# Performance work log

Hardware: AMD Instinct MI355X
Metric: run time of the kernel (lower is better)

The kernel has to match this reference:

```python
import jax, jax.numpy as jnp
import numpy as np
from jax import lax

H, P, N, G, K, CHUNK = 64, 64, 128, 1, 4, 256
D_MODEL = 2048
D_INNER = H * P            # 4096
CONV_DIM = D_INNER + 2 * G * N  # 4352
EPS = 1e-5


def setup_inputs() -> dict:
    key = jax.random.key(0)
    ks = jax.random.split(key, 6)
    s = lambda k, shape, scale: jax.random.normal(k, shape, jnp.float32) * scale
    return {
        "hidden_states": s(ks[0], (2, 2048, D_MODEL), 1.0),
        "in_proj_w": s(ks[1], (D_MODEL, D_INNER + CONV_DIM + H), D_MODEL ** -0.5),
        "conv_w": s(ks[2], (CONV_DIM, K), K ** -0.5),
        "conv_b": jnp.zeros((CONV_DIM,), jnp.float32),
        "dt_bias": jnp.ones((H,), jnp.float32),
        "A_log": jnp.log(jnp.arange(1, H + 1, dtype=jnp.float32)),
        "D_param": jnp.ones((H,), jnp.float32),
        "norm_w": jnp.ones((D_INNER,), jnp.float32),
        "out_proj_w": s(ks[3], (D_INNER, D_MODEL), D_INNER ** -0.5),
    }


def _mamba2_forward(hidden_states, in_proj_w, conv_w, conv_b, dt_bias, A_log, D_param, norm_w, out_proj_w):
    b, l, _ = hidden_states.shape
    c = l // CHUNK  # number of chunks

    # in_proj -> gate | conv channels (x,B,C) | dt
    proj = hidden_states @ in_proj_w
    gate = proj[..., :D_INNER]
    hbc = proj[..., D_INNER:D_INNER + CONV_DIM]
    dt = proj[..., D_INNER + CONV_DIM:]  # [b,l,H]

    # depthwise causal conv1d + silu
    xt = hbc.transpose(0, 2, 1)  # [b, CONV_DIM, l]
    y = lax.conv_general_dilated(
        xt, conv_w[:, None, :], window_strides=(1,), padding=[(K - 1, 0)],
        feature_group_count=CONV_DIM, dimension_numbers=("NCH", "OIH", "NCH"))
    hbc = jax.nn.silu(y + conv_b[None, :, None]).transpose(0, 2, 1)  # [b,l,CONV_DIM]

    # split into x / B / C per group (unflatten over groups as in torch code)
    per_g = D_INNER // G
    hg = hbc.reshape(b, l, G, per_g + 2 * N)
    x = hg[..., :per_g].reshape(b, l, H, P)                 # [b,l,h,p]
    Bm = hg[..., per_g:per_g + N]                            # [b,l,g,n]
    Cm = hg[..., per_g + N:]                                 # [b,l,g,n]
    hpg = H // G
    Bh = jnp.repeat(Bm, hpg, axis=2)                         # [b,l,h,n]
    Ch = jnp.repeat(Cm, hpg, axis=2)

    # dt: softplus(dt + bias), clamp per time_step_limit (0, inf)
    dt = jax.nn.softplus(dt + dt_bias)                       # [b,l,h]
    A = -jnp.exp(A_log)                                      # [h]

    # chunk the sequence
    x_c = x.reshape(b, c, CHUNK, H, P)
    B_c = Bh.reshape(b, c, CHUNK, H, N)
    C_c = Ch.reshape(b, c, CHUNK, H, N)
    dt_c = dt.reshape(b, c, CHUNK, H)

    dA = dt_c * A[None, None, None, :]                       # [b,c,L,h]
    cum = jnp.cumsum(dA, axis=2)                             # [b,c,L,h]

    # intra-chunk (diagonal block): decay[i,j] = exp(cum_i - cum_j), i>=j
    diff = cum[:, :, :, None, :] - cum[:, :, None, :, :]     # [b,c,i,j,h]
    i = jnp.arange(CHUNK)
    mask = i[:, None] >= i[None, :]
    decay = jnp.exp(jnp.where(mask[None, None, :, :, None], diff, -jnp.inf))
    scores = jnp.einsum("bcihn,bcjhn->bcijh", C_c, B_c) * decay * dt_c[:, :, None, :, :]
    Y_diag = jnp.einsum("bcijh,bcjhp->bcihp", scores, x_c)   # [b,c,L,h,p]

    # per-chunk final states
    decay_states = jnp.exp(cum[:, :, -1:, :] - cum)          # [b,c,L,h]
    states = jnp.einsum("bclh,bclhn,bclhp->bchpn", decay_states * dt_c, B_c, x_c)
    chunk_decay = jnp.exp(cum[:, :, -1, :])                  # [b,c,h]

    # inter-chunk recurrence over chunks
    def step(prev, inp):
        st, cd = inp  # [b,h,p,n], [b,h]
        new = cd[:, :, None, None] * prev + st
        return new, prev

    init = jnp.zeros((b, H, P, N), hidden_states.dtype)
    _, prev_states = lax.scan(step, init, (jnp.moveaxis(states, 1, 0), jnp.moveaxis(chunk_decay, 1, 0)))
    prev_states = jnp.moveaxis(prev_states, 0, 1)            # [b,c,h,p,n]

    state_decay_out = jnp.exp(cum)                           # [b,c,L,h]
    Y_off = jnp.einsum("bclhn,bchpn,bclh->bclhp", C_c, prev_states, state_decay_out)

    yh = (Y_diag + Y_off).reshape(b, l, H, P) + D_param[None, None, :, None] * x
    yr = yh.reshape(b, l, D_INNER)

    # gated RMSNorm
    hidden = yr * jax.nn.silu(gate)
    var = jnp.mean(hidden * hidden, axis=-1, keepdims=True)
    hidden = hidden * lax.rsqrt(var + EPS) * norm_w

    return hidden @ out_proj_w


def reference(hidden_states, in_proj_w, conv_w, conv_b, dt_bias, A_log, D_param, norm_w, out_proj_w):
    return _mamba2_forward(hidden_states, in_proj_w, conv_w, conv_b, dt_bias, A_log, D_param, norm_w, out_proj_w)
```

## Files before the change

### kernel.cpp

```cpp
#include <hip/hip_runtime.h>
#include <hip/hip_bf16.h>


typedef __attribute__((ext_vector_type(8))) _Float16 f16x8;
typedef __attribute__((ext_vector_type(4))) float f32x4;

#define GLD16(gp, lp) __builtin_amdgcn_global_load_lds( \
    (__attribute__((address_space(1))) void*)(gp),      \
    (__attribute__((address_space(3))) void*)(lp), 16, 0, 0)

__device__ __forceinline__ unsigned short f2h(float v) {
  _Float16 h = (_Float16)v;
  return *reinterpret_cast<unsigned short*>(&h);
}
__device__ __forceinline__ float h2f(unsigned short u) {
  _Float16 h = *reinterpret_cast<_Float16*>(&u);
  return (float)h;
}
__device__ __forceinline__ float siluf(float x) { return x / (1.f + expf(-x)); }

__global__ __launch_bounds__(256) void prep(const float* __restrict__ hs,
                                            const float* __restrict__ Win,
                                            _Float16* __restrict__ Ah,
                                            _Float16* __restrict__ WtH,
                                            float* __restrict__ zf) {
  __shared__ __attribute__((aligned(16))) char smemP[32768];
  const int bid = blockIdx.x;
  const int tid = threadIdx.x;
  if (bid < 1024) {
    float (*Xs)[2048] = reinterpret_cast<float (*)[2048]>(smemP);
    int t0 = bid * 4;
#pragma unroll
    for (int i = 0; i < 8; i++) {
      int e = tid * 4 + i * 1024;
      int tok = e >> 11, k = e & 2047;
      *reinterpret_cast<float4*>(&Xs[tok][k]) =
          *reinterpret_cast<const float4*>(&hs[(long)(t0 + tok) * 2048 + k]);
    }
    __syncthreads();
    int h = tid & 63, tg = tid >> 6;
    float a0 = 0.f, a1 = 0.f, a2 = 0.f, a3 = 0.f;
    const float* wcol = Win + 8448 + h;
    for (int k = 0; k < 2048; k += 4) {
      a0 = fmaf(Xs[tg][k + 0], wcol[(long)(k + 0) * 8512], a0);
      a1 = fmaf(Xs[tg][k + 1], wcol[(long)(k + 1) * 8512], a1);
      a2 = fmaf(Xs[tg][k + 2], wcol[(long)(k + 2) * 8512], a2);
      a3 = fmaf(Xs[tg][k + 3], wcol[(long)(k + 3) * 8512], a3);
    }
    zf[(long)(t0 + tg) * 64 + h] = (a0 + a1) + (a2 + a3);
  } else if (bid < 9216) {
    long i = ((long)(bid - 1024) * 256 + tid) * 4;
    float4 v = *reinterpret_cast<const float4*>(hs + i);
    ushort4 u;
    u.x = f2h(v.x); u.y = f2h(v.y); u.z = f2h(v.z); u.w = f2h(v.w);
    *reinterpret_cast<ushort4*>((unsigned short*)Ah + i) = u;
  } else {
    float (*tile)[33] = reinterpret_cast<float (*)[33]>(smemP);
    int i = bid - 9216;
    int c0 = (i % 264) * 32, r0 = (i / 264) * 32;
    int tx = tid & 31, ty = tid >> 5;
#pragma unroll
    for (int j = 0; j < 4; j++)
      tile[ty + j * 8][tx] = Win[(long)(r0 + ty + j * 8) * 8512 + c0 + tx];
    __syncthreads();
#pragma unroll
    for (int j = 0; j < 4; j++) {
      int c = c0 + ty + j * 8, r = r0 + tx;
      WtH[(long)c * 2048 + r] = (_Float16)tile[tx][ty + j * 8];
    }
  }
}

__global__ __launch_bounds__(512, 2) void gemm_in8(const _Float16* __restrict__ A,
                                                   const _Float16* __restrict__ Bt,
                                                   _Float16* __restrict__ gate,
                                                   float* __restrict__ hbcf,
                                                   float* __restrict__ rparts) {
  __shared__ __attribute__((aligned(128))) char ldsB[131072];
  const int tid = threadIdx.x;
  const int lane = tid & 63;
  const int wv = tid >> 6;
  const int wr = wv >> 2, wc = wv & 3;
  const int wg = blockIdx.x;
  const bool rem = wg >= 512;
  int by, bxn, kbase, zz;
  if (!rem) {
    const int xcd = wg & 7, j = wg >> 3;
    by = (xcd >> 2) * 8 + (j >> 3);
    bxn = (xcd & 3) * 8 + (j & 7);
    kbase = 0; zz = 0;
  } else {
    const int idx = wg - 512;
    by = idx & 15; zz = idx >> 4; bxn = 32; kbase = zz * 256;
  }

  const int srow = tid >> 3;
  const int scolg = (tid & 7) ^ (srow & 7);
  const _Float16* Ab = A + (long)by * 524288 + (long)srow * 2048 + scolg * 8 + kbase;
  const _Float16* Bb = Bt + (long)bxn * 524288 + (long)srow * 2048 + scolg * 8 + kbase;
  const int ldst = tid << 4;

#define STAGE_A(tau, h) do {                                              \
    const _Float16* g_ = Ab + (long)(h) * 262144 + (tau) * 64;            \
    char* l_ = ldsB + ((((tau) & 1) << 2) + (h)) * 16384 + ldst;          \
    GLD16(g_, l_); GLD16(g_ + 131072, l_ + 8192); } while (0)
#define STAGE_B(tau, h) do {                                              \
    const _Float16* g_ = Bb + (long)(h) * 262144 + (tau) * 64;            \
    char* l_ = ldsB + ((((tau) & 1) << 2) + 2 + (h)) * 16384 + ldst;      \
    GLD16(g_, l_); GLD16(g_ + 131072, l_ + 8192); } while (0)

  const int fr = lane & 15;
  const int c16 = (lane >> 4) ^ (fr & 7);
  const int aOff0 = wr * 16384 + fr * 128 + c16 * 16;
  const int aOff1 = aOff0 ^ 64;
  const int bOff0 = (2 + (wc >> 1)) * 16384 + ((wc & 1) * 64 + fr) * 128 + c16 * 16;
  const int bOff1 = bOff0 ^ 64;
#define RD_A(b, mi, k32) (*(const f16x8*)(ldsB + ((k32) ? aOff1 : aOff0) + (b) * 65536 + (mi) * 2048))
#define RD_B(b, ni, k32) (*(const f16x8*)(ldsB + ((k32) ? bOff1 : bOff0) + (b) * 65536 + (ni) * 2048))

#define BAR() __builtin_amdgcn_s_barrier()
#define WLG0() asm volatile("s_waitcnt lgkmcnt(0)" ::: "memory")
#define WLG8() asm volatile("s_waitcnt lgkmcnt(8)" ::: "memory")
#define WVM4() asm volatile("s_waitcnt vmcnt(4)" ::: "memory")

  f32x4 acc[8][4];
#pragma unroll
  for (int mi = 0; mi < 8; ++mi)
#pragma unroll
    for (int ni = 0; ni < 4; ++ni) acc[mi][ni] = f32x4{0.f, 0.f, 0.f, 0.f};

  STAGE_A(0, 0); STAGE_A(0, 1); STAGE_B(0, 0); STAGE_B(0, 1);
  STAGE_B(1, 0); STAGE_B(1, 1);
  WVM4(); BAR();

#define MFMA_Q(MI0, MI1, x0, x1, x2, x3, PB)                                        \
  __builtin_amdgcn_s_setprio(1);                                                    \
  _Pragma("unroll") for (int ni = 0; ni < 4; ++ni) {                                \
    acc[MI0][ni] = __builtin_amdgcn_mfma_f32_16x16x32_f16(x0, PB[ni][0], acc[MI0][ni], 0, 0, 0); \
    acc[MI0][ni] = __builtin_amdgcn_mfma_f32_16x16x32_f16(x1, PB[ni][1], acc[MI0][ni], 0, 0, 0); \
    acc[MI1][ni] = __builtin_amdgcn_mfma_f32_16x16x32_f16(x2, PB[ni][0], acc[MI1][ni], 0, 0, 0); \
    acc[MI1][ni] = __builtin_amdgcn_mfma_f32_16x16x32_f16(x3, PB[ni][1], acc[MI1][ni], 0, 0, 0); \
  }                                                                                 \
  __builtin_amdgcn_s_setprio(0);

#define ITER8(u, msk) do {                                                          \
    const int t1 = (2 * (u) + 1) & (msk);                                           \
    const int t2 = (2 * (u) + 2) & (msk);                                           \
    const int t3 = (2 * (u) + 3) & (msk);                                           \
    f16x8 PB0[4][2];                                                                \
    _Pragma("unroll") for (int ni = 0; ni < 4; ++ni) {                              \
      PB0[ni][0] = RD_B(0, ni, 0); PB0[ni][1] = RD_B(0, ni, 1); }                   \
    {                                                                               \
      f16x8 x0 = RD_A(0, 0, 0), x1 = RD_A(0, 0, 1), x2 = RD_A(0, 1, 0), x3 = RD_A(0, 1, 1); \
      STAGE_A(t1, 0); WLG8(); BAR(); WLG0();                                        \
      MFMA_Q(0, 1, x0, x1, x2, x3, PB0) BAR();                                      \
    }                                                                               \
    {                                                                               \
      f16x8 x0 = RD_A(0, 2, 0), x1 = RD_A(0, 2, 1), x2 = RD_A(0, 3, 0), x3 = RD_A(0, 3, 1); \
      STAGE_A(t1, 1); BAR(); WLG0();                                                \
      MFMA_Q(2, 3, x0, x1, x2, x3, PB0) BAR();                                      \
    }                                                                               \
    {                                                                               \
      f16x8 x0 = RD_A(0, 4, 0), x1 = RD_A(0, 4, 1), x2 = RD_A(0, 5, 0), x3 = RD_A(0, 5, 1); \
      STAGE_B(t2, 0); BAR(); WLG0();                                                \
      MFMA_Q(4, 5, x0, x1, x2, x3, PB0) BAR();                                      \
    }                                                                               \
    {                                                                               \
      f16x8 x0 = RD_A(0, 6, 0), x1 = RD_A(0, 6, 1), x2 = RD_A(0, 7, 0), x3 = RD_A(0, 7, 1); \
      STAGE_B(t2, 1); BAR(); WLG0();                                                \
      MFMA_Q(6, 7, x0, x1, x2, x3, PB0) WVM4(); BAR();                              \
    }                                                                               \
    f16x8 PB1[4][2];                                                                \
    _Pragma("unroll") for (int ni = 0; ni < 4; ++ni) {                              \
      PB1[ni][0] = RD_B(1, ni, 0); PB1[ni][1] = RD_B(1, ni, 1); }                   \
    {                                                                               \
      f16x8 x0 = RD_A(1, 0, 0), x1 = RD_A(1, 0, 1), x2 = RD_A(1, 1, 0), x3 = RD_A(1, 1, 1); \
      STAGE_A(t2, 0); WLG8(); BAR(); WLG0();                                        \
      MFMA_Q(0, 1, x0, x1, x2, x3, PB1) BAR();                                      \
    }                                                                               \
    {                                                                               \
      f16x8 x0 = RD_A(1, 2, 0), x1 = RD_A(1, 2, 1), x2 = RD_A(1, 3, 0), x3 = RD_A(1, 3, 1); \
      STAGE_A(t2, 1); BAR(); WLG0();                                                \
      MFMA_Q(2, 3, x0, x1, x2, x3, PB1) BAR();                                      \
    }                                                                               \
    {                                                                               \
      f16x8 x0 = RD_A(1, 4, 0), x1 = RD_A(1, 4, 1), x2 = RD_A(1, 5, 0), x3 = RD_A(1, 5, 1); \
      STAGE_B(t3, 0); BAR(); WLG0();                                                \
      MFMA_Q(4, 5, x0, x1, x2, x3, PB1) BAR();                                      \
    }                                                                               \
    {                                                                               \
      f16x8 x0 = RD_A(1, 6, 0), x1 = RD_A(1, 6, 1), x2 = RD_A(1, 7, 0), x3 = RD_A(1, 7, 1); \
      STAGE_B(t3, 1); BAR(); WLG0();                                                \
      MFMA_Q(6, 7, x0, x1, x2, x3, PB1) WVM4(); BAR();                              \
    }                                                                               \
  } while (0)

  if (!rem) {
    for (int u = 0; u < 16; ++u) ITER8(u, 31);
  } else {
    for (int u = 0; u < 2; ++u) ITER8(u, 3);
  }

  const int m0 = by * 256 + wr * 128;
  const int cl = lane & 15, rq = (lane >> 4) * 4;
  if (!rem) {
    const int n0 = bxn * 256 + wc * 64;
    if (bxn < 16) {
#pragma unroll
      for (int mi = 0; mi < 8; ++mi)
#pragma unroll
        for (int r = 0; r < 4; ++r) {
          long rowoff = (long)(m0 + mi * 16 + rq + r) * 4096 + n0 + cl;
#pragma unroll
          for (int ni = 0; ni < 4; ++ni) gate[rowoff + ni * 16] = (_Float16)acc[mi][ni][r];
        }
    } else {
#pragma unroll
      for (int mi = 0; mi < 8; ++mi)
#pragma unroll
        for (int r = 0; r < 4; ++r) {
          long rowoff = (long)(m0 + mi * 16 + rq + r) * 4352 + (n0 - 4096) + cl;
#pragma unroll
          for (int ni = 0; ni < 4; ++ni) hbcf[rowoff + ni * 16] = acc[mi][ni][r];
        }
    }
  } else {
    float* rp = rparts + (long)zz * 1048576;
    const int ncol = wc * 64;
#pragma unroll
    for (int mi = 0; mi < 8; ++mi)
#pragma unroll
      for (int r = 0; r < 4; ++r) {
        long rowoff = (long)(m0 + mi * 16 + rq + r) * 256 + ncol + cl;
#pragma unroll
        for (int ni = 0; ni < 4; ++ni) rp[rowoff + ni * 16] = acc[mi][ni][r];
      }
  }
#undef STAGE_A
#undef STAGE_B
#undef RD_A
#undef RD_B
#undef ITER8
}

__global__ __launch_bounds__(256) void fuse2(const float* __restrict__ zf,
                                             const float* __restrict__ dtb,
                                             const float* __restrict__ Alog,
                                             float* __restrict__ dt_f,
                                             float* __restrict__ cum_f,
                                             float* __restrict__ cuml,
                                             const float* __restrict__ rp,
                                             float* __restrict__ hbcf,
                                             const float* __restrict__ Wout,
                                             _Float16* __restrict__ WoutT) {
  __shared__ __attribute__((aligned(16))) char smem2[4352];
  const int bid = blockIdx.x;
  const int tid = threadIdx.x;
  if (bid < 16) {
    float (*segsum)[64] = reinterpret_cast<float (*)[64]>(smem2);
    int bc = bid;
    int h = tid & 63, seg = tid >> 6;
    int t0 = bc * 256;
    float Ah = -expf(Alog[h]);
    float bias = dtb[h];
    float s = 0.f;
    for (int j = 0; j < 64; j++) {
      int t = t0 + seg * 64 + j;
      float z = zf[(long)t * 64 + h] + bias;
      float v = (z > 20.f) ? z : log1pf(expf(z));
      dt_f[(long)t * 64 + h] = v;
      s += v * Ah;
    }
    segsum[seg][h] = s;
    __syncthreads();
    float run = 0.f;
    for (int k = 0; k < seg; k++) run += segsum[k][h];
    for (int j = 0; j < 64; j++) {
      int t = t0 + seg * 64 + j;
      run += dt_f[(long)t * 64 + h] * Ah;
      cum_f[(long)t * 64 + h] = run;
    }
    if (seg == 3) cuml[bc * 64 + h] = run;
  } else if (bid < 1040) {
    long e = ((long)(bid - 16) * 256 + tid) * 4;
    float4 s = *reinterpret_cast<const float4*>(rp + e);
#pragma unroll
    for (int z = 1; z < 8; ++z) {
      float4 v = *reinterpret_cast<const float4*>(rp + (long)z * 1048576 + e);
      s.x += v.x; s.y += v.y; s.z += v.z; s.w += v.w;
    }
    long row = e >> 8, col = e & 255;
    *reinterpret_cast<float4*>(hbcf + row * 4352 + 4096 + col) = s;
  } else {
    float (*tile)[33] = reinterpret_cast<float (*)[33]>(smem2);
    int i = bid - 1040;
    int c0 = (i & 63) * 32, r0 = (i >> 6) * 32;
    int tx = tid & 31, ty = tid >> 5;
#pragma unroll
    for (int j = 0; j < 4; j++)
      tile[ty + j * 8][tx] = Wout[(long)(r0 + ty + j * 8) * 2048 + c0 + tx];
    __syncthreads();
#pragma unroll
    for (int j = 0; j < 4; j++) {
      int c = c0 + ty + j * 8, r = r0 + tx;
      WoutT[(long)c * 4096 + r] = (_Float16)tile[tx][ty + j * 8];
    }
  }
}

__global__ __launch_bounds__(256) void convx(const float* __restrict__ hbcf,
                                             const float* __restrict__ convw,
                                             const float* __restrict__ convb,
                                             _Float16* __restrict__ x16,
                                             _Float16* __restrict__ B16,
                                             _Float16* __restrict__ C16,
                                             unsigned short* __restrict__ xT16) {
  __shared__ unsigned short tile[64][66];
  const int bx = blockIdx.x, t0 = blockIdx.y * 64;
  const int tid = threadIdx.x;
  const int tq = tid & 63, tg = tid >> 6;
  const int q0 = (bx < 64) ? bx * 64 : 4096 + (bx - 64) * 64;
  const int q = q0 + tq;
  const int ts = t0 + tg * 16;
  const int bstart = ts & ~2047;
  const float* colq = hbcf + q;
  float4 wq = *reinterpret_cast<const float4*>(convw + q * 4);
  float bconv = convb[q];
  float v3 = (ts - 3 >= bstart) ? colq[(long)(ts - 3) * 4352] : 0.f;
  float v2 = (ts - 2 >= bstart) ? colq[(long)(ts - 2) * 4352] : 0.f;
  float v1 = (ts - 1 >= bstart) ? colq[(long)(ts - 1) * 4352] : 0.f;
  if (bx < 64) {
#pragma unroll
    for (int j = 0; j < 16; ++j) {
      int t = ts + j;
      float v0 = colq[(long)t * 4352];
      float a = bconv + v3 * wq.x + v2 * wq.y + v1 * wq.z + v0 * wq.w;
      unsigned short o = f2h(siluf(a));
      ((unsigned short*)x16)[(long)t * 4096 + q] = o;
      tile[tg * 16 + j][tq] = o;
      v3 = v2; v2 = v1; v1 = v0;
    }
    __syncthreads();
    int tx = tid & 15, ty = tid >> 4;
#pragma unroll
    for (int i = 0; i < 4; ++i) {
      int c = ty + i * 16;
      ushort4 v;
      v.x = tile[4 * tx + 0][c]; v.y = tile[4 * tx + 1][c];
      v.z = tile[4 * tx + 2][c]; v.w = tile[4 * tx + 3][c];
      *(ushort4*)&xT16[(long)(q0 + c) * 4096 + t0 + 4 * tx] = v;
    }
  } else {
#pragma unroll
    for (int j = 0; j < 16; ++j) {
      int t = ts + j;
      float v0 = colq[(long)t * 4352];
      float a = bconv + v3 * wq.x + v2 * wq.y + v1 * wq.z + v0 * wq.w;
      _Float16 o = (_Float16)siluf(a);
      if (q < 4224) B16[(long)t * 128 + (q - 4096)] = o;
      else C16[(long)t * 128 + (q - 4224)] = o;
      v3 = v2; v2 = v1; v1 = v0;
    }
  }
}

__global__ __launch_bounds__(256) void fuse3(const unsigned short* __restrict__ xT16,
                                             const _Float16* __restrict__ B16,
                                             const _Float16* __restrict__ C16,
                                             const float* __restrict__ dt_f,
                                             const float* __restrict__ cum_f,
                                             const float* __restrict__ cuml,
                                             float* __restrict__ states,
                                             float* __restrict__ CBT,
                                             float* __restrict__ ssq) {
  __shared__ __attribute__((aligned(16))) char smem3[16384];
  const int bid = blockIdx.x;
  const int tid = threadIdx.x;
  const int wv = tid >> 6, lane = tid & 63;
  const int mr = lane & 15, koff = (lane >> 4) * 8;
  if (bid < 1024) {
    float* w_s = (float*)smem3;
    unsigned short* Aw = (unsigned short*)(smem3 + 1024);
    unsigned short* BT = (unsigned short*)(smem3 + 6144);
    int h = bid & 63, bc = bid >> 6;
    int t0 = bc * 256;
    {
      int t = t0 + tid;
      w_s[tid] = expf(cuml[bc * 64 + h] - cum_f[(long)t * 64 + h]) * dt_f[(long)t * 64 + h];
    }
    __syncthreads();
    f32x4 acc[4][2];
#pragma unroll
    for (int mi = 0; mi < 4; mi++)
#pragma unroll
      for (int nj = 0; nj < 2; nj++) acc[mi][nj] = f32x4{0.f, 0.f, 0.f, 0.f};
    for (int kt = 0; kt < 8; kt++) {
      {
        int p = tid >> 2, tq2 = tid & 3;
        const unsigned short* g = &xT16[((long)(h * 64 + p)) * 4096 + t0 + kt * 32 + tq2 * 8];
        ushort4 u0 = *(const ushort4*)g, u1 = *(const ushort4*)(g + 4);
        const float* wp = &w_s[kt * 32 + tq2 * 8];
        ushort4 o0, o1;
        o0.x = f2h(h2f(u0.x) * wp[0]); o0.y = f2h(h2f(u0.y) * wp[1]);
        o0.z = f2h(h2f(u0.z) * wp[2]); o0.w = f2h(h2f(u0.w) * wp[3]);
        o1.x = f2h(h2f(u1.x) * wp[4]); o1.y = f2h(h2f(u1.y) * wp[5]);
        o1.z = f2h(h2f(u1.z) * wp[6]); o1.w = f2h(h2f(u1.w) * wp[7]);
        *(ushort4*)&Aw[p * 40 + tq2 * 8] = o0;
        *(ushort4*)&Aw[p * 40 + tq2 * 8 + 4] = o1;
      }
      {
        int tl = tid >> 3, ng = tid & 7;
        const unsigned short* g = (const unsigned short*)B16 +
                                  ((long)(t0 + kt * 32 + tl)) * 128 + ng * 16;
#pragma unroll
        for (int j = 0; j < 16; j++) BT[(ng * 16 + j) * 40 + tl] = g[j];
      }
      __syncthreads();
      f16x8 af[4], bf[2];
#pragma unroll
      for (int mi = 0; mi < 4; mi++)
        af[mi] = *(const f16x8*)&Aw[(mi * 16 + mr) * 40 + koff];
#pragma unroll
      for (int nj = 0; nj < 2; nj++)
        bf[nj] = *(const f16x8*)&BT[((wv * 2 + nj) * 16 + mr) * 40 + koff];
#pragma unroll
      for (int mi = 0; mi < 4; mi++)
#pragma unroll
        for (int nj = 0; nj < 2; nj++)
          acc[mi][nj] = __builtin_amdgcn_mfma_f32_16x16x32_f16(af[mi], bf[nj],
                                                               acc[mi][nj], 0, 0, 0);
      __syncthreads();
    }
    int cl = lane & 15, rq = (lane >> 4) * 4;
    long base = ((long)(bc * 64 + h)) * 8192;
#pragma unroll
    for (int mi = 0; mi < 4; mi++)
#pragma unroll
      for (int r = 0; r < 4; r++) {
        int p = mi * 16 + rq + r;
#pragma unroll
        for (int nj = 0; nj < 2; nj++) {
          int n = (wv * 2 + nj) * 16 + cl;
          states[base + p * 128 + n] = acc[mi][nj][r];
        }
      }
  } else if (bid < 1088) {
    _Float16* As = (_Float16*)smem3;
    _Float16* Bs = (_Float16*)(smem3 + 8192);
    int i = bid - 1024;
    int bx = i & 1, by = (i >> 1) & 1, bz = i >> 2;
    const _Float16* Ab = C16 + (long)bz * 32768 + (long)by * 128 * 128;
    const _Float16* Bb = B16 + (long)bz * 32768 + (long)bx * 128 * 128;
    const int c0 = wv * 128 + lane;
    const int c1 = c0 + 64;
    const long ra0 = (long)(c0 >> 2) * 128 + (c0 & 3) * 8;
    const long ra1 = (long)(c1 >> 2) * 128 + (c1 & 3) * 8;
    f32x4 acc[4][4];
#pragma unroll
    for (int mi = 0; mi < 4; mi++)
#pragma unroll
      for (int ni = 0; ni < 4; ni++) acc[mi][ni] = f32x4{0.f, 0.f, 0.f, 0.f};
    const int mrow = (wv & 1) * 64 + (lane & 15);
    const int nrow = (wv >> 1) * 64 + (lane & 15);
    for (int k0 = 0; k0 < 128; k0 += 32) {
      GLD16(Ab + ra0 + k0, (char*)As + c0 * 16);
      GLD16(Ab + ra1 + k0, (char*)As + c1 * 16);
      GLD16(Bb + ra0 + k0, (char*)Bs + c0 * 16);
      GLD16(Bb + ra1 + k0, (char*)Bs + c1 * 16);
      __syncthreads();
      f16x8 af[4], bfr[4];
#pragma unroll
      for (int mi = 0; mi < 4; mi++)
        af[mi] = *(const f16x8*)(As + (mrow + mi * 16) * 32 + koff);
#pragma unroll
      for (int ni = 0; ni < 4; ni++)
        bfr[ni] = *(const f16x8*)(Bs + (nrow + ni * 16) * 32 + koff);
#pragma unroll
      for (int mi = 0; mi < 4; mi++)
#pragma unroll
        for (int ni = 0; ni < 4; ni++)
          acc[mi][ni] = __builtin_amdgcn_mfma_f32_16x16x32_f16(af[mi], bfr[ni],
                                                               acc[mi][ni], 0, 0, 0);
      __syncthreads();
    }
    const int m0 = by * 128 + (wv & 1) * 64;
    const int n0 = bx * 128 + (wv >> 1) * 64;
    const int cl = lane & 15, rq = (lane >> 4) * 4;
    const long zc = (long)bz * 65536;
#pragma unroll
    for (int mi = 0; mi < 4; mi++)
#pragma unroll
      for (int r = 0; r < 4; r++) {
        long rowoff = zc + (long)(m0 + mi * 16 + rq + r) * 256 + n0 + cl;
#pragma unroll
        for (int ni = 0; ni < 4; ni++) CBT[rowoff + ni * 16] = acc[mi][ni][r];
      }
  } else {
    int i = (bid - 1088) * 1024 + tid * 4;
    *reinterpret_cast<float4*>(&ssq[i]) = make_float4(0.f, 0.f, 0.f, 0.f);
  }
}

__global__ __launch_bounds__(256) void recur_kernel(float* __restrict__ states,
                                                    const float* __restrict__ cuml) {
  int g = blockIdx.x;
  int bh = g >> 3, js = g & 7;
  int b = bh >> 6, h = bh & 63;
  int tid = threadIdx.x;
  float4 prev = make_float4(0.f, 0.f, 0.f, 0.f);
  for (int c = 0; c < 8; c++) {
    int bc = b * 8 + c;
    float cd = expf(cuml[bc * 64 + h]);
    long o = (long)(bc * 64 + h) * 8192 + js * 1024 + tid * 4;
    float4 st = *reinterpret_cast<const float4*>(&states[o]);
    *reinterpret_cast<float4*>(&states[o]) = prev;
    prev.x = fmaf(cd, prev.x, st.x);
    prev.y = fmaf(cd, prev.y, st.y);
    prev.z = fmaf(cd, prev.z, st.z);
    prev.w = fmaf(cd, prev.w, st.w);
  }
}

__global__ __launch_bounds__(256, 4) void yfused(const unsigned short* __restrict__ xT16,
                                                 const unsigned short* __restrict__ x16,
                                                 const unsigned short* __restrict__ C16,
                                                 const unsigned short* __restrict__ gate,
                                                 const float* __restrict__ CBT,
                                                 const float* __restrict__ states,
                                                 const float* __restrict__ dt_f,
                                                 const float* __restrict__ cum_f,
                                                 const float* __restrict__ Dp,
                                                 unsigned short* __restrict__ hid,
                                                 float* __restrict__ ssq) {
  int h = blockIdx.x, bc = blockIdx.y;
  int t0 = bc * 256, tid = threadIdx.x;
  __shared__ unsigned short Sb[256 * 40];
  __shared__ unsigned short PS[64 * 136];
  __shared__ float cum_s[256], dt_s[256];
  int i = tid;
  cum_s[i] = cum_f[(long)(t0 + i) * 64 + h];
  dt_s[i] = dt_f[(long)(t0 + i) * 64 + h];
  {
    int p = tid >> 2, nq = tid & 3;
    const float* g = &states[((long)(bc * 64 + h)) * 8192 + p * 128 + nq * 32];
    unsigned short* l = &PS[p * 136 + nq * 32];
#pragma unroll
    for (int c = 0; c < 8; c++) {
      float4 v = *(const float4*)(g + c * 4);
      ushort4 u;
      u.x = f2h(v.x); u.y = f2h(v.y); u.z = f2h(v.z); u.w = f2h(v.w);
      *(ushort4*)(l + c * 4) = u;
    }
  }
  __syncthreads();
  float cum_i = cum_s[i];
  const float* cbrow = CBT + (long)bc * 65536 + (long)i * 256;
  int wv = tid >> 6, lane = tid & 63;
  int mr = lane & 15, koff = (lane >> 4) * 8;
  const unsigned short* xTb = xT16 + ((long)(h * 64 + mr)) * 4096 + t0 + koff;
  f32x4 acc[4][4];
#pragma unroll
  for (int mi = 0; mi < 4; mi++)
#pragma unroll
    for (int ni = 0; ni < 4; ni++) acc[mi][ni] = f32x4{0.f, 0.f, 0.f, 0.f};
  const int ktmax = 2 * wv + 2;
  for (int kt = 0; kt < ktmax; kt++) {
    int k0 = kt * 32;
    f16x8 bf[4];
#pragma unroll
    for (int ni = 0; ni < 4; ni++)
      bf[ni] = *(const f16x8*)(xTb + (long)(ni * 16) * 4096 + k0);
#pragma unroll
    for (int c = 0; c < 8; c++) {
      float4 cb = *(const float4*)&cbrow[k0 + c * 4];
      ushort4 o;
      {
        int j = k0 + c * 4 + 0;
        float s = (j <= i) ? cb.x * expf(cum_i - cum_s[j]) * dt_s[j] : 0.f;
        o.x = f2h(s);
      }
      {
        int j = k0 + c * 4 + 1;
        float s = (j <= i) ? cb.y * expf(cum_i - cum_s[j]) * dt_s[j] : 0.f;
        o.y = f2h(s);
      }
      {
        int j = k0 + c * 4 + 2;
        float s = (j <= i) ? cb.z * expf(cum_i - cum_s[j]) * dt_s[j] : 0.f;
        o.z = f2h(s);
      }
      {
        int j = k0 + c * 4 + 3;
        float s = (j <= i) ? cb.w * expf(cum_i - cum_s[j]) * dt_s[j] : 0.f;
        o.w = f2h(s);
      }
      *(ushort4*)&Sb[i * 40 + c * 4] = o;
    }
    f16x8 af[4];
#pragma unroll
    for (int mi = 0; mi < 4; mi++)
      af[mi] = *(const f16x8*)&Sb[(64 * wv + mi * 16 + mr) * 40 + koff];
#pragma unroll
    for (int mi = 0; mi < 4; mi++)
#pragma unroll
      for (int ni = 0; ni < 4; ni++)
        acc[mi][ni] = __builtin_amdgcn_mfma_f32_16x16x32_f16(af[mi], bf[ni],
                                                             acc[mi][ni], 0, 0, 0);
  }
  float fac_i = expf(cum_i);
  for (int kn = 0; kn < 4; kn++) {
    {
      const unsigned short* g = &C16[((long)(t0 + i)) * 128 + kn * 32];
#pragma unroll
      for (int c = 0; c < 8; c++) {
        ushort4 u = *(const ushort4*)(g + c * 4);
        ushort4 o;
        o.x = f2h(h2f(u.x) * fac_i); o.y = f2h(h2f(u.y) * fac_i);
        o.z = f2h(h2f(u.z) * fac_i); o.w = f2h(h2f(u.w) * fac_i);
        *(ushort4*)&Sb[i * 40 + c * 4] = o;
      }
    }
    f16x8 af[4], bf[4];
#pragma unroll
    for (int mi = 0; mi < 4; mi++)
      af[mi] = *(const f16x8*)&Sb[(64 * wv + mi * 16 + mr) * 40 + koff];
#pragma unroll
    for (int ni = 0; ni < 4; ni++)
      bf[ni] = *(const f16x8*)&PS[(ni * 16 + mr) * 136 + kn * 32 + koff];
#pragma unroll
    for (int mi = 0; mi < 4; mi++)
#pragma unroll
      for (int ni = 0; ni < 4; ni++)
        acc[mi][ni] = __builtin_amdgcn_mfma_f32_16x16x32_f16(af[mi], bf[ni],
                                                             acc[mi][ni], 0, 0, 0);
  }
  float Dh = Dp[h];
  int cl = lane & 15, rq = (lane >> 4) * 4;
#pragma unroll
  for (int mi = 0; mi < 4; mi++)
#pragma unroll
    for (int r = 0; r < 4; r++) {
      long row = t0 + 64 * wv + mi * 16 + rq + r;
      const unsigned short* xr = &x16[row * 4096 + h * 64];
      const unsigned short* gr = &gate[row * 4096 + h * 64];
      unsigned short* hw = &hid[row * 4096 + h * 64];
      float ssp = 0.f;
#pragma unroll
      for (int ni = 0; ni < 4; ni++) {
        int p = ni * 16 + cl;
        float yv = acc[mi][ni][r] + Dh * h2f(xr[p]);
        float hv = yv * siluf(h2f(gr[p]));
        hw[p] = f2h(hv);
        ssp += hv * hv;
      }
#pragma unroll
      for (int o = 8; o > 0; o >>= 1) ssp += __shfl_down(ssp, o, 16);
      if (cl == 0) atomicAdd(&ssq[row], ssp);
    }
}

__global__ __launch_bounds__(256) void scale_kernel(const float* __restrict__ ssq,
                                                    const float* __restrict__ nw,
                                                    unsigned short* __restrict__ hid) {
  int row = blockIdx.x;
  int tid = threadIdx.x;
  float sc = rsqrtf(ssq[row] * (1.f / 4096.f) + 1e-5f);
  unsigned short* hp = hid + (long)row * 4096;
  int d0 = tid * 16;
#pragma unroll
  for (int c = 0; c < 4; c++) {
    int d = d0 + c * 4;
    ushort4 u = *reinterpret_cast<ushort4*>(&hp[d]);
    float4 w = *reinterpret_cast<const float4*>(&nw[d]);
    u.x = f2h(h2f(u.x) * sc * w.x);
    u.y = f2h(h2f(u.y) * sc * w.y);
    u.z = f2h(h2f(u.z) * sc * w.z);
    u.w = f2h(h2f(u.w) * sc * w.w);
    *reinterpret_cast<ushort4*>(&hp[d]) = u;
  }
}

__global__ __launch_bounds__(512, 2) void gemm_out8(const _Float16* __restrict__ A,
                                                    const _Float16* __restrict__ Bt,
                                                    float* __restrict__ Cp0,
                                                    float* __restrict__ Cp1) {
  __shared__ __attribute__((aligned(128))) char ldsB[131072];
  const int tid = threadIdx.x;
  const int lane = tid & 63;
  const int wv = tid >> 6;
  const int wr = wv >> 2, wc = wv & 3;
  const int wg = blockIdx.x;
  const int xcd = wg & 7, j = wg >> 3;
  const int z = j >> 4, t = j & 15;
  const int by = (xcd >> 1) * 4 + (t >> 2);
  const int bx = (xcd & 1) * 4 + (t & 3);

  const int srow = tid >> 3;
  const int scolg = (tid & 7) ^ (srow & 7);
  const _Float16* Ab = A + (long)by * 256 * 4096 + (long)z * 2048 +
                       (long)srow * 4096 + scolg * 8;
  const _Float16* Bb = Bt + (long)bx * 256 * 4096 + (long)z * 2048 +
                       (long)srow * 4096 + scolg * 8;
  const int ldst = tid << 4;

#define STAGE_A(tau, h) do {                                              \
    const _Float16* g_ = Ab + (long)(h) * 524288 + (tau) * 64;            \
    char* l_ = ldsB + ((((tau) & 1) << 2) + (h)) * 16384 + ldst;          \
    GLD16(g_, l_); GLD16(g_ + 262144, l_ + 8192); } while (0)
#define STAGE_B(tau, h) do {                                              \
    const _Float16* g_ = Bb + (long)(h) * 524288 + (tau) * 64;            \
    char* l_ = ldsB + ((((tau) & 1) << 2) + 2 + (h)) * 16384 + ldst;      \
    GLD16(g_, l_); GLD16(g_ + 262144, l_ + 8192); } while (0)

  const int fr = lane & 15;
  const int c16 = (lane >> 4) ^ (fr & 7);
  const int aOff0 = wr * 16384 + fr * 128 + c16 * 16;
  const int aOff1 = aOff0 ^ 64;
  const int bOff0 = (2 + (wc >> 1)) * 16384 + ((wc & 1) * 64 + fr) * 128 + c16 * 16;
  const int bOff1 = bOff0 ^ 64;
#define RD_A(b, mi, k32) (*(const f16x8*)(ldsB + ((k32) ? aOff1 : aOff0) + (b) * 65536 + (mi) * 2048))
#define RD_B(b, ni, k32) (*(const f16x8*)(ldsB + ((k32) ? bOff1 : bOff0) + (b) * 65536 + (ni) * 2048))

#define BAR() __builtin_amdgcn_s_barrier()
#define WLG0() asm volatile("s_waitcnt lgkmcnt(0)" ::: "memory")
#define WLG8() asm volatile("s_waitcnt lgkmcnt(8)" ::: "memory")
#define WVM4() asm volatile("s_waitcnt vmcnt(4)" ::: "memory")

  f32x4 acc[8][4];
#pragma unroll
  for (int mi = 0; mi < 8; ++mi)
#pragma unroll
    for (int ni = 0; ni < 4; ++ni) acc[mi][ni] = f32x4{0.f, 0.f, 0.f, 0.f};

  STAGE_A(0, 0); STAGE_A(0, 1); STAGE_B(0, 0); STAGE_B(0, 1);
  STAGE_B(1, 0); STAGE_B(1, 1);
  WVM4(); BAR();

#define MFMA_Q(MI0, MI1, x0, x1, x2, x3, PB)                                        \
  __builtin_amdgcn_s_setprio(1);                                                    \
  _Pragma("unroll") for (int ni = 0; ni < 4; ++ni) {                                \
    acc[MI0][ni] = __builtin_amdgcn_mfma_f32_16x16x32_f16(x0, PB[ni][0], acc[MI0][ni], 0, 0, 0); \
    acc[MI0][ni] = __builtin_amdgcn_mfma_f32_16x16x32_f16(x1, PB[ni][1], acc[MI0][ni], 0, 0, 0); \
    acc[MI1][ni] = __builtin_amdgcn_mfma_f32_16x16x32_f16(x2, PB[ni][0], acc[MI1][ni], 0, 0, 0); \
    acc[MI1][ni] = __builtin_amdgcn_mfma_f32_16x16x32_f16(x3, PB[ni][1], acc[MI1][ni], 0, 0, 0); \
  }                                                                                 \
  __builtin_amdgcn_s_setprio(0);

  for (int u = 0; u < 16; ++u) {
    const int t1 = 2 * u + 1;
    const int t2 = (2 * u + 2) & 31;
    const int t3 = (2 * u + 3) & 31;
    f16x8 PB0[4][2];
#pragma unroll
    for (int ni = 0; ni < 4; ++ni) { PB0[ni][0] = RD_B(0, ni, 0); PB0[ni][1] = RD_B(0, ni, 1); }
    {
      f16x8 x0 = RD_A(0, 0, 0), x1 = RD_A(0, 0, 1), x2 = RD_A(0, 1, 0), x3 = RD_A(0, 1, 1);
      STAGE_A(t1, 0); WLG8(); BAR(); WLG0();
      MFMA_Q(0, 1, x0, x1, x2, x3, PB0) BAR();
    }
    {
      f16x8 x0 = RD_A(0, 2, 0), x1 = RD_A(0, 2, 1), x2 = RD_A(0, 3, 0), x3 = RD_A(0, 3, 1);
      STAGE_A(t1, 1); BAR(); WLG0();
      MFMA_Q(2, 3, x0, x1, x2, x3, PB0) BAR();
    }
    {
      f16x8 x0 = RD_A(0, 4, 0), x1 = RD_A(0, 4, 1), x2 = RD_A(0, 5, 0), x3 = RD_A(0, 5, 1);
      STAGE_B(t2, 0); BAR(); WLG0();
      MFMA_Q(4, 5, x0, x1, x2, x3, PB0) BAR();
    }
    {
      f16x8 x0 = RD_A(0, 6, 0), x1 = RD_A(0, 6, 1), x2 = RD_A(0, 7, 0), x3 = RD_A(0, 7, 1);
      STAGE_B(t2, 1); BAR(); WLG0();
      MFMA_Q(6, 7, x0, x1, x2, x3, PB0) WVM4(); BAR();
    }
    f16x8 PB1[4][2];
#pragma unroll
    for (int ni = 0; ni < 4; ++ni) { PB1[ni][0] = RD_B(1, ni, 0); PB1[ni][1] = RD_B(1, ni, 1); }
    {
      f16x8 x0 = RD_A(1, 0, 0), x1 = RD_A(1, 0, 1), x2 = RD_A(1, 1, 0), x3 = RD_A(1, 1, 1);
      STAGE_A(t2, 0); WLG8(); BAR(); WLG0();
      MFMA_Q(0, 1, x0, x1, x2, x3, PB1) BAR();
    }
    {
      f16x8 x0 = RD_A(1, 2, 0), x1 = RD_A(1, 2, 1), x2 = RD_A(1, 3, 0), x3 = RD_A(1, 3, 1);
      STAGE_A(t2, 1); BAR(); WLG0();
      MFMA_Q(2, 3, x0, x1, x2, x3, PB1) BAR();
    }
    {
      f16x8 x0 = RD_A(1, 4, 0), x1 = RD_A(1, 4, 1), x2 = RD_A(1, 5, 0), x3 = RD_A(1, 5, 1);
      STAGE_B(t3, 0); BAR(); WLG0();
      MFMA_Q(4, 5, x0, x1, x2, x3, PB1) BAR();
    }
    {
      f16x8 x0 = RD_A(1, 6, 0), x1 = RD_A(1, 6, 1), x2 = RD_A(1, 7, 0), x3 = RD_A(1, 7, 1);
      STAGE_B(t3, 1); BAR(); WLG0();
      MFMA_Q(6, 7, x0, x1, x2, x3, PB1) WVM4(); BAR();
    }
  }
  const int m0 = by * 256 + wr * 128;
  const int n0 = bx * 256 + wc * 64;
  const int cl = lane & 15, rq = (lane >> 4) * 4;
  float* Cb = z ? Cp1 : Cp0;
#pragma unroll
  for (int mi = 0; mi < 8; ++mi)
#pragma unroll
    for (int r = 0; r < 4; ++r) {
      long rowoff = (long)(m0 + mi * 16 + rq + r) * 2048 + n0 + cl;
#pragma unroll
      for (int ni = 0; ni < 4; ++ni) Cb[rowoff + ni * 16] = acc[mi][ni][r];
    }
#undef STAGE_A
#undef STAGE_B
#undef RD_A
#undef RD_B
#undef BAR
#undef WLG0
#undef WLG8
#undef WVM4
#undef MFMA_Q
}

__global__ __launch_bounds__(256) void add_out(const float* __restrict__ p0,
                                               const float* __restrict__ p1,
                                               float* __restrict__ o) {
  long i = ((long)blockIdx.x * 256 + threadIdx.x) * 4;
  float4 a = *reinterpret_cast<const float4*>(p0 + i);
  float4 b = *reinterpret_cast<const float4*>(p1 + i);
  float4 r;
  r.x = a.x + b.x; r.y = a.y + b.y; r.z = a.z + b.z; r.w = a.w + b.w;
  *reinterpret_cast<float4*>(o + i) = r;
}

extern "C" void kernel_launch(void* const* d_in, const int* in_sizes, int n_in,
                              void* d_out, int out_size, void* d_ws, size_t ws_size,
                              hipStream_t stream) {
  (void)in_sizes; (void)n_in; (void)out_size; (void)ws_size;
  const float* hs    = (const float*)d_in[0];
  const float* Win   = (const float*)d_in[1];
  const float* convw = (const float*)d_in[2];
  const float* convb = (const float*)d_in[3];
  const float* dtb   = (const float*)d_in[4];
  const float* Alog  = (const float*)d_in[5];
  const float* Dp    = (const float*)d_in[6];
  const float* nw    = (const float*)d_in[7];
  const float* Wout  = (const float*)d_in[8];
  float* out = (float*)d_out;

  char* base = (char*)d_ws;
  size_t off = 0;
  auto take = [&](size_t n) { char* r = base + off; off += (n + 255) & ~(size_t)255; return r; };
  float*    hbcf  = (float*)take(4096UL * 4352 * 4);
  _Float16* gateh = (_Float16*)take(4096UL * 4096 * 2);
  _Float16* Ah    = (_Float16*)take(4096UL * 2048 * 2);
  _Float16* WtH   = (_Float16*)take(8448UL * 2048 * 2);
  _Float16* xT16  = (_Float16*)take(4096UL * 4096 * 2);
  _Float16* B16   = (_Float16*)take(4096UL * 128 * 2);
  _Float16* C16   = (_Float16*)take(4096UL * 128 * 2);
  float*    zf    = (float*)take(4096UL * 64 * 4);
  float*    dt_f  = (float*)take(4096UL * 64 * 4);
  float*    cum_f = (float*)take(4096UL * 64 * 4);
  float*    cuml  = (float*)take(16UL * 64 * 4);
  float*    ssq   = (float*)take(4096UL * 4);
  float*    CBT   = (float*)take(16UL * 256 * 256 * 4);
  float*    states= (float*)take(1024UL * 8192 * 4);
  float*    rparts = states;
  _Float16* WoutT  = Ah;
  _Float16* x16    = WtH;
  unsigned short* hid = (unsigned short*)hbcf;
  float*    oparts0 = states;
  float*    oparts1 = (float*)gateh;

  prep<<<26112, 256, 0, stream>>>(hs, Win, Ah, WtH, zf);
  gemm_in8<<<dim3(640), 512, 0, stream>>>(Ah, WtH, gateh, hbcf, rparts);
  fuse2<<<9232, 256, 0, stream>>>(zf, dtb, Alog, dt_f, cum_f, cuml,
                                  rparts, hbcf, Wout, WoutT);
  convx<<<dim3(68, 64), 256, 0, stream>>>(hbcf, convw, convb, x16, B16, C16,
                                          (unsigned short*)xT16);
  fuse3<<<1092, 256, 0, stream>>>((const unsigned short*)xT16, B16, C16,
                                  dt_f, cum_f, cuml, states, CBT, ssq);
  recur_kernel<<<1024, 256, 0, stream>>>(states, cuml);
  yfused<<<dim3(64, 16), 256, 0, stream>>>((const unsigned short*)xT16,
                                           (const unsigned short*)x16,
                                           (const unsigned short*)C16,
                                           (const unsigned short*)gateh,
                                           CBT, states, dt_f, cum_f, Dp,
                                           hid, ssq);
  scale_kernel<<<4096, 256, 0, stream>>>(ssq, nw, hid);
  gemm_out8<<<dim3(256), 512, 0, stream>>>((const _Float16*)hid, WoutT,
                                           oparts0, oparts1);
  add_out<<<8192, 256, 0, stream>>>(oparts0, oparts1, out);
}
```

Before: 710.7 us.

## Transpose CB product layout, stage x tile in LDS, use exp2 in yfused

The CB GEMM now swaps its operands so it produces the transposed matrix. Each thread in yfused then reads its column with coalesced loads across threads, where it previously read a strided row with float4 loads. The x-transposed tile for the chunk is preloaded into LDS once instead of being fetched from global memory on each k iteration. The cumsum is prescaled by log2(e) so exp2f replaces expf, and the occupancy hint in the launch bounds is dropped. In exchange, LDS use grows by about 33KB, which may lower occupancy.

After: 701.2 us. Within noise of the previous version (-1.3%).

```diff
diff --git a/kernel.cpp b/kernel.cpp
--- a/kernel.cpp
+++ b/kernel.cpp
@@ -449,8 +449,8 @@
     _Float16* Bs = (_Float16*)(smem3 + 8192);
     int i = bid - 1024;
     int bx = i & 1, by = (i >> 1) & 1, bz = i >> 2;
-    const _Float16* Ab = C16 + (long)bz * 32768 + (long)by * 128 * 128;
-    const _Float16* Bb = B16 + (long)bz * 32768 + (long)bx * 128 * 128;
+    const _Float16* Ab = B16 + (long)bz * 32768 + (long)by * 128 * 128;
+    const _Float16* Bb = C16 + (long)bz * 32768 + (long)bx * 128 * 128;
     const int c0 = wv * 128 + lane;
     const int c1 = c0 + 64;
     const long ra0 = (long)(c0 >> 2) * 128 + (c0 & 3) * 8;
@@ -521,25 +521,34 @@
   }
 }
 
-__global__ __launch_bounds__(256, 4) void yfused(const unsigned short* __restrict__ xT16,
-                                                 const unsigned short* __restrict__ x16,
-                                                 const unsigned short* __restrict__ C16,
-                                                 const unsigned short* __restrict__ gate,
-                                                 const float* __restrict__ CBT,
-                                                 const float* __restrict__ states,
-                                                 const float* __restrict__ dt_f,
-                                                 const float* __restrict__ cum_f,
-                                                 const float* __restrict__ Dp,
-                                                 unsigned short* __restrict__ hid,
-                                                 float* __restrict__ ssq) {
+__global__ __launch_bounds__(256) void yfused(const unsigned short* __restrict__ xT16,
+                                              const unsigned short* __restrict__ x16,
+                                              const unsigned short* __restrict__ C16,
+                                              const unsigned short* __restrict__ gate,
+                                              const float* __restrict__ CBTt,
+                                              const float* __restrict__ states,
+                                              const float* __restrict__ dt_f,
+                                              const float* __restrict__ cum_f,
+                                              const float* __restrict__ Dp,
+                                              unsigned short* __restrict__ hid,
+                                              float* __restrict__ ssq) {
   int h = blockIdx.x, bc = blockIdx.y;
   int t0 = bc * 256, tid = threadIdx.x;
   __shared__ unsigned short Sb[256 * 40];
+  __shared__ unsigned short Xb[64 * 264];
   __shared__ unsigned short PS[64 * 136];
-  __shared__ float cum_s[256], dt_s[256];
+  __shared__ float c2_s[256], dt_s[256];
   int i = tid;
-  cum_s[i] = cum_f[(long)(t0 + i) * 64 + h];
+  c2_s[i] = cum_f[(long)(t0 + i) * 64 + h] * 1.44269504f;
   dt_s[i] = dt_f[(long)(t0 + i) * 64 + h];
+  {
+    int p = tid >> 2, tq = tid & 3;
+    const unsigned short* g = &xT16[((long)(h * 64 + p)) * 4096 + t0 + tq * 64];
+    unsigned short* l = &Xb[p * 264 + tq * 64];
+#pragma unroll
+    for (int c = 0; c < 8; c++)
+      *(uint4*)(l + c * 8) = *(const uint4*)(g + c * 8);
+  }
   {
     int p = tid >> 2, nq = tid & 3;
     const float* g = &states[((long)(bc * 64 + h)) * 8192 + p * 128 + nq * 32];
@@ -553,11 +562,10 @@
     }
   }
   __syncthreads();
-  float cum_i = cum_s[i];
-  const float* cbrow = CBT + (long)bc * 65536 + (long)i * 256;
+  float c2_i = c2_s[i];
+  const float* cbcol = CBTt + (long)bc * 65536 + i;
   int wv = tid >> 6, lane = tid & 63;
   int mr = lane & 15, koff = (lane >> 4) * 8;
-  const unsigned short* xTb = xT16 + ((long)(h * 64 + mr)) * 4096 + t0 + koff;
   f32x4 acc[4][4];
 #pragma unroll
   for (int mi = 0; mi < 4; mi++)
@@ -566,40 +574,27 @@
   const int ktmax = 2 * wv + 2;
   for (int kt = 0; kt < ktmax; kt++) {
     int k0 = kt * 32;
-    f16x8 bf[4];
-#pragma unroll
-    for (int ni = 0; ni < 4; ni++)
-      bf[ni] = *(const f16x8*)(xTb + (long)(ni * 16) * 4096 + k0);
 #pragma unroll
     for (int c = 0; c < 8; c++) {
-      float4 cb = *(const float4*)&cbrow[k0 + c * 4];
+      int jb = k0 + c * 4;
+      float cb0 = cbcol[(long)(jb + 0) * 256];
+      float cb1 = cbcol[(long)(jb + 1) * 256];
+      float cb2 = cbcol[(long)(jb + 2) * 256];
+      float cb3 = cbcol[(long)(jb + 3) * 256];
       ushort4 o;
-      {
-        int j = k0 + c * 4 + 0;
-        float s = (j <= i) ? cb.x * expf(cum_i - cum_s[j]) * dt_s[j] : 0.f;
-        o.x = f2h(s);
-      }
-      {
-        int j = k0 + c * 4 + 1;
-        float s = (j <= i) ? cb.y * expf(cum_i - cum_s[j]) * dt_s[j] : 0.f;
-        o.y = f2h(s);
-      }
-      {
-        int j = k0 + c * 4 + 2;
-        float s = (j <= i) ? cb.z * expf(cum_i - cum_s[j]) * dt_s[j] : 0.f;
-        o.z = f2h(s);
-      }
-      {
-        int j = k0 + c * 4 + 3;
-        float s = (j <= i) ? cb.w * expf(cum_i - cum_s[j]) * dt_s[j] : 0.f;
-        o.w = f2h(s);
-      }
+      o.x = f2h((jb + 0 <= i) ? cb0 * exp2f(c2_i - c2_s[jb + 0]) * dt_s[jb + 0] : 0.f);
+      o.y = f2h((jb + 1 <= i) ? cb1 * exp2f(c2_i - c2_s[jb + 1]) * dt_s[jb + 1] : 0.f);
+      o.z = f2h((jb + 2 <= i) ? cb2 * exp2f(c2_i - c2_s[jb + 2]) * dt_s[jb + 2] : 0.f);
+      o.w = f2h((jb + 3 <= i) ? cb3 * exp2f(c2_i - c2_s[jb + 3]) * dt_s[jb + 3] : 0.f);
       *(ushort4*)&Sb[i * 40 + c * 4] = o;
     }
-    f16x8 af[4];
+    f16x8 af[4], bf[4];
 #pragma unroll
     for (int mi = 0; mi < 4; mi++)
       af[mi] = *(const f16x8*)&Sb[(64 * wv + mi * 16 + mr) * 40 + koff];
+#pragma unroll
+    for (int ni = 0; ni < 4; ni++)
+      bf[ni] = *(const f16x8*)&Xb[(ni * 16 + mr) * 264 + k0 + koff];
 #pragma unroll
     for (int mi = 0; mi < 4; mi++)
 #pragma unroll
@@ -607,7 +602,7 @@
         acc[mi][ni] = __builtin_amdgcn_mfma_f32_16x16x32_f16(af[mi], bf[ni],
                                                              acc[mi][ni], 0, 0, 0);
   }
-  float fac_i = expf(cum_i);
+  float fac_i = exp2f(c2_i);
   for (int kn = 0; kn < 4; kn++) {
     {
       const unsigned short* g = &C16[((long)(t0 + i)) * 128 + kn * 32];
```
